# Kernel optimization log

Hardware: AMD Instinct MI355X
Metric: run time of the kernel (lower is better)

The kernel has to match this reference:

```python
import jax, jax.numpy as jnp
import numpy as np

IN_FEATURES = 4096
OUT_FEATURES = 16384

def setup_inputs() -> dict:
    key = jax.random.key(0)
    k1, k2 = jax.random.split(key)
    x = jax.random.normal(k1, (4, 2048, IN_FEATURES), dtype=jnp.float32)
    # init_weights: uniform(-1, 1)
    W = jax.random.uniform(k2, (OUT_FEATURES, IN_FEATURES), dtype=jnp.float32, minval=-1.0, maxval=1.0)
    b = jnp.zeros((OUT_FEATURES,), dtype=jnp.float32)
    return {"x": x, "W": W, "b": b}

def reference(x, W, b):
    # Binarize weights to {-1, 0, +1} via sign, then dense linear: y = x @ sign(W)^T + b
    Wb = jnp.sign(W)
    return jnp.einsum('bsd,od->bso', x, Wb) + b
```

## Files before the change

### kernel.cpp

```cpp
#include <hip/hip_runtime.h>
#include <hip/hip_bf16.h>

#define M_TOT 8192
#define N_TOT 16384
#define K_TOT 4096
#define NT (K_TOT / 64)

typedef int i32x4 __attribute__((ext_vector_type(4)));
typedef int i32x16 __attribute__((ext_vector_type(16)));
typedef __bf16 bf16x8 __attribute__((ext_vector_type(8)));
typedef float f32x4 __attribute__((ext_vector_type(4)));

#define GLOAD_LDS16(g, l)                                                     \
  __builtin_amdgcn_global_load_lds(                                           \
      (__attribute__((address_space(1))) const void*)(g),                     \
      (__attribute__((address_space(3))) void*)(l), 16, 0, 0)

__device__ __forceinline__ ushort f2bf_rne(float f) {
  unsigned u = __float_as_uint(f);
  u += 0x7FFFu + ((u >> 16) & 1u);
  return (ushort)(u >> 16);
}
__device__ __forceinline__ ushort sgn_bf16(float w) {
  return w > 0.f ? (ushort)0x3F80u : (w < 0.f ? (ushort)0xBF80u : (ushort)0u);
}


__global__ void quant_x_kernel(const float* __restrict__ x,
                               char* __restrict__ At, float* __restrict__ s) {
  int row = blockIdx.x;
  int tid = threadIdx.x;
  const float4* xr = (const float4*)(x + (size_t)row * K_TOT + tid * 16);
  float4 v[4];
  float amax = 0.f;
#pragma unroll
  for (int j = 0; j < 4; ++j) {
    v[j] = xr[j];
    amax = fmaxf(amax, fmaxf(fmaxf(fabsf(v[j].x), fabsf(v[j].y)),
                             fmaxf(fabsf(v[j].z), fabsf(v[j].w))));
  }
#pragma unroll
  for (int o = 32; o > 0; o >>= 1) amax = fmaxf(amax, __shfl_xor(amax, o));
  __shared__ float wmax[4];
  if ((tid & 63) == 0) wmax[tid >> 6] = amax;
  __syncthreads();
  amax = fmaxf(fmaxf(wmax[0], wmax[1]), fmaxf(wmax[2], wmax[3]));
  float inv = amax > 0.f ? 127.0f / amax : 0.f;
  if (tid == 0) s[row] = amax * (1.0f / 127.0f);
  int q[16];
#pragma unroll
  for (int j = 0; j < 4; ++j) {
    q[j * 4 + 0] = max(-127, min(127, __float2int_rn(v[j].x * inv)));
    q[j * 4 + 1] = max(-127, min(127, __float2int_rn(v[j].y * inv)));
    q[j * 4 + 2] = max(-127, min(127, __float2int_rn(v[j].z * inv)));
    q[j * 4 + 3] = max(-127, min(127, __float2int_rn(v[j].w * inv)));
  }
  int4 o4;
  int* op = (int*)&o4;
#pragma unroll
  for (int j = 0; j < 4; ++j)
    op[j] = (q[j * 4] & 255) | ((q[j * 4 + 1] & 255) << 8) |
            ((q[j * 4 + 2] & 255) << 16) | ((q[j * 4 + 3] & 255) << 24);
  int r32 = row >> 5, l31 = row & 31;
  int kt = tid >> 2, ks = (tid >> 1) & 1, hi = tid & 1;
  size_t dst = ((size_t)(r32 * 128 + kt * 2 + ks) << 10) + ((hi * 32 + l31) << 4);
  *(int4*)(At + dst) = o4;
}

__global__ void quant_w_kernel(const float* __restrict__ w,
                               char* __restrict__ Bt) {
  int n32 = blockIdx.x;
  int t = threadIdx.x;
#pragma unroll 4
  for (int i = 0; i < 32; ++i) {
    int c = i * 256 + t;
    int kt = c >> 7, ks = (c >> 6) & 1, l = c & 63;
    int n = n32 * 32 + (l & 31);
    int k = kt * 64 + ks * 32 + (l >> 5) * 16;
    const float4* src = (const float4*)(w + (size_t)n * K_TOT + k);
    int4 o4;
    int* op = (int*)&o4;
#pragma unroll
    for (int j = 0; j < 4; ++j) {
      float4 v = src[j];
      int q0 = v.x > 0.f ? 1 : (v.x < 0.f ? -1 : 0);
      int q1 = v.y > 0.f ? 1 : (v.y < 0.f ? -1 : 0);
      int q2 = v.z > 0.f ? 1 : (v.z < 0.f ? -1 : 0);
      int q3 = v.w > 0.f ? 1 : (v.w < 0.f ? -1 : 0);
      op[j] = (q0 & 255) | ((q1 & 255) << 8) | ((q2 & 255) << 16) |
              ((q3 & 255) << 24);
    }
    *(int4*)(Bt + ((size_t)n32 << 17) + ((size_t)c << 4)) = o4;
  }
}

__global__ __launch_bounds__(512, 2) void gemm_i8_big4(
    const char* __restrict__ At, const char* __restrict__ Bt,
    const float* __restrict__ s, const float* __restrict__ bias,
    float* __restrict__ C) {
  __shared__ char lds[4][32768];

  int bid = blockIdx.x;
  int wg = (bid & 7) * 256 + (bid >> 3);
  int bnS = wg >> 8;
  int rem = wg & 255;
  int bm = rem >> 3;
  int bn = bnS * 8 + (rem & 7);
  int rowBase = bm * 256;
  int colBase = bn * 256;

  int t = threadIdx.x;
  int lane = t & 63;
  int wave = t >> 6;
  int wr = wave >> 2;
  int wc = wave & 3;
  int l31 = lane & 31;
  int hi = lane >> 5;

  const char* gAp[2];
  const char* gBp[2];
#pragma unroll
  for (int q = 0; q < 2; ++q) {
    int ss = t + 512 * q;
    int g = ss >> 6;
    int r32l = g >> 1, ks = g & 1;
    int j = ss & 63;
    gAp[q] = At + ((size_t)((bm * 8 + r32l) * 128 + ks) << 10) + (j << 4);
    gBp[q] = Bt + ((size_t)((bn * 8 + r32l) * 128 + ks) << 10) + (j << 4);
  }

  i32x16 acc[4][2] = {};

#define STAGE(kt_, buf_)                                                      \
  {                                                                           \
    size_t _o = (size_t)(kt_) << 11;                                          \
    GLOAD_LDS16(gAp[0] + _o, &lds[buf_][t * 16]);                             \
    GLOAD_LDS16(gAp[1] + _o, &lds[buf_][8192 + t * 16]);                      \
    GLOAD_LDS16(gBp[0] + _o, &lds[buf_][16384 + t * 16]);                     \
    GLOAD_LDS16(gBp[1] + _o, &lds[buf_][24576 + t * 16]);                     \
  }
#define COMPUTE(buf_)                                                         \
  {                                                                           \
    const char* _la = &lds[buf_][0];                                          \
    const char* _lb = _la + 16384;                                            \
    _Pragma("unroll") for (int ks = 0; ks < 2; ++ks) {                        \
      i32x4 bf0 = *(const i32x4*)(_lb + (((wc * 2 + 0) * 2 + ks) << 10) +     \
                                  (lane << 4));                               \
      i32x4 bf1 = *(const i32x4*)(_lb + (((wc * 2 + 1) * 2 + ks) << 10) +     \
                                  (lane << 4));                               \
      _Pragma("unroll") for (int mi = 0; mi < 4; ++mi) {                      \
        i32x4 _af = *(const i32x4*)(_la + (((wr * 4 + mi) * 2 + ks) << 10) +  \
                                    (lane << 4));                             \
        acc[mi][0] = __builtin_amdgcn_mfma_i32_32x32x32_i8(                   \
            _af, bf0, acc[mi][0], 0, 0, 0);                                   \
        acc[mi][1] = __builtin_amdgcn_mfma_i32_32x32x32_i8(                   \
            _af, bf1, acc[mi][1], 0, 0, 0);                                   \
      }                                                                       \
    }                                                                         \
  }

  STAGE(0, 0);
  STAGE(1, 1);
  asm volatile("s_waitcnt vmcnt(4)" ::: "memory");
  __builtin_amdgcn_sched_barrier(0);
  __builtin_amdgcn_s_barrier();
  __builtin_amdgcn_sched_barrier(0);

  for (int tt = 0; tt < NT; ++tt) {
    int buf = tt & 3;
    if (tt + 2 < NT) {
      STAGE(tt + 2, (tt + 2) & 3);
      asm volatile("s_waitcnt vmcnt(4)" ::: "memory");
    } else if (tt + 1 < NT) {
      asm volatile("s_waitcnt vmcnt(0)" ::: "memory");
    }
    COMPUTE(buf);
    __builtin_amdgcn_sched_barrier(0);
    __builtin_amdgcn_s_barrier();
    __builtin_amdgcn_sched_barrier(0);
  }

#undef COMPUTE
#undef STAGE

#pragma unroll
  for (int mi = 0; mi < 4; ++mi) {
#pragma unroll
    for (int ni = 0; ni < 2; ++ni) {
      int gc = colBase + wc * 64 + ni * 32 + l31;
      float bv = bias[gc];
#pragma unroll
      for (int rg = 0; rg < 16; ++rg) {
        int rowIn = (rg & 3) + 8 * (rg >> 2) + 4 * hi;
        int gr = rowBase + wr * 128 + mi * 32 + rowIn;
        C[(size_t)gr * N_TOT + gc] = (float)acc[mi][ni][rg] * s[gr] + bv;
      }
    }
  }
}

__global__ void gemm_fused_kernel(const float* __restrict__ A,
                                  const float* __restrict__ W,
                                  const float* __restrict__ bias,
                                  float* __restrict__ C) {
  __shared__ ushort lsA[128 * 32];
  __shared__ ushort lsB[128 * 32];

  int nwg = gridDim.x;
  int bid = blockIdx.x;
  int wg = (bid & 7) * (nwg >> 3) + (bid >> 3);
  const int NBN = N_TOT / 128;
  int bm = wg / NBN;
  int bn = wg % NBN;
  int rowBase = bm * 128;
  int colBase = bn * 128;

  int t = threadIdx.x;
  int lane = t & 63;
  int wave = t >> 6;
  int wm = (wave >> 1) * 64;
  int wn = (wave & 1) * 64;

  f32x4 acc[4][4] = {};

  int srow = t >> 3;
  int scol = (t & 7) * 4;
  int fr = lane & 15;
  int koff = (lane >> 4) * 8;

  for (int k0 = 0; k0 < K_TOT; k0 += 32) {
    float4 va[4], vb[4];
#pragma unroll
    for (int r = 0; r < 4; ++r) {
      va[r] = *(const float4*)&A[(size_t)(rowBase + r * 32 + srow) * K_TOT + k0 + scol];
      vb[r] = *(const float4*)&W[(size_t)(colBase + r * 32 + srow) * K_TOT + k0 + scol];
    }
    __syncthreads();
#pragma unroll
    for (int r = 0; r < 4; ++r) {
      int e = r * 1024 + t * 4;
      ushort4 oa, ob;
      oa.x = f2bf_rne(va[r].x); oa.y = f2bf_rne(va[r].y);
      oa.z = f2bf_rne(va[r].z); oa.w = f2bf_rne(va[r].w);
      ob.x = sgn_bf16(vb[r].x); ob.y = sgn_bf16(vb[r].y);
      ob.z = sgn_bf16(vb[r].z); ob.w = sgn_bf16(vb[r].w);
      *(ushort4*)&lsA[e] = oa;
      *(ushort4*)&lsB[e] = ob;
    }
    __syncthreads();

    bf16x8 af[4], bfr[4];
#pragma unroll
    for (int i = 0; i < 4; ++i)
      af[i] = *(const bf16x8*)&lsA[(wm + i * 16 + fr) * 32 + koff];
#pragma unroll
    for (int j = 0; j < 4; ++j)
      bfr[j] = *(const bf16x8*)&lsB[(wn + j * 16 + fr) * 32 + koff];

#pragma unroll
    for (int i = 0; i < 4; ++i)
#pragma unroll
      for (int j = 0; j < 4; ++j)
        acc[i][j] = __builtin_amdgcn_mfma_f32_16x16x32_bf16(af[i], bfr[j],
                                                            acc[i][j], 0, 0, 0);
  }

  int orow0 = rowBase + wm + ((lane >> 4) << 2);
  int ocol0 = colBase + wn + (lane & 15);
#pragma unroll
  for (int i = 0; i < 4; ++i) {
#pragma unroll
    for (int j = 0; j < 4; ++j) {
      int col = ocol0 + j * 16;
      float bv = bias[col];
#pragma unroll
      for (int rg = 0; rg < 4; ++rg) {
        int row = orow0 + i * 16 + rg;
        C[(size_t)row * N_TOT + col] = acc[i][j][rg] + bv;
      }
    }
  }
}

extern "C" void kernel_launch(void* const* d_in, const int* in_sizes, int n_in,
                              void* d_out, int out_size, void* d_ws,
                              size_t ws_size, hipStream_t stream) {
  const float* x = (const float*)d_in[0];
  const float* W = (const float*)d_in[1];
  const float* b = (const float*)d_in[2];
  float* out = (float*)d_out;

  const size_t xq_bytes = (size_t)M_TOT * K_TOT;
  const size_t wq_bytes = (size_t)N_TOT * K_TOT;
  const size_t need = xq_bytes + wq_bytes + M_TOT * 4;

  if (ws_size >= need) {
    char* At = (char*)d_ws;
    char* Bt = At + xq_bytes;
    float* s = (float*)(Bt + wq_bytes);
    quant_x_kernel<<<M_TOT, 256, 0, stream>>>(x, At, s);
    quant_w_kernel<<<N_TOT / 32, 256, 0, stream>>>(W, Bt);
    const int nblocks = (M_TOT / 256) * (N_TOT / 256);
    gemm_i8_big4<<<nblocks, 512, 0, stream>>>(At, Bt, s, b, out);
  } else {
    const int nblocks = (M_TOT / 128) * (N_TOT / 128);
    gemm_fused_kernel<<<nblocks, 256, 0, stream>>>(x, W, b, out);
  }
}
```

Baseline: 679.9 us.

## Use 4 fat waves with 128x128 warp tiles in int8 GEMM

```diff
diff --git a/kernel.cpp b/kernel.cpp
--- a/kernel.cpp
+++ b/kernel.cpp
@@ -94,7 +94,7 @@
   }
 }
 
-__global__ __launch_bounds__(512, 2) void gemm_i8_big4(
+__global__ __launch_bounds__(256, 1) void gemm_i8_fat(
     const char* __restrict__ At, const char* __restrict__ Bt,
     const float* __restrict__ s, const float* __restrict__ bias,
     float* __restrict__ C) {
@@ -112,56 +112,60 @@
   int t = threadIdx.x;
   int lane = t & 63;
   int wave = t >> 6;
-  int wr = wave >> 2;
-  int wc = wave & 3;
+  int wr = wave >> 1;
+  int wc = wave & 1;
   int l31 = lane & 31;
   int hi = lane >> 5;
 
-  const char* gAp[2];
-  const char* gBp[2];
-#pragma unroll
-  for (int q = 0; q < 2; ++q) {
-    int ss = t + 512 * q;
-    int g = ss >> 6;
+  const char* gp[8];
+#pragma unroll
+  for (int q = 0; q < 8; ++q) {
+    int ss = t + 256 * q;
+    int g = (ss >> 6) & 15;
     int r32l = g >> 1, ks = g & 1;
     int j = ss & 63;
-    gAp[q] = At + ((size_t)((bm * 8 + r32l) * 128 + ks) << 10) + (j << 4);
-    gBp[q] = Bt + ((size_t)((bn * 8 + r32l) * 128 + ks) << 10) + (j << 4);
-  }
-
-  i32x16 acc[4][2] = {};
+    const char* base =
+        (q < 4) ? At + ((size_t)((bm * 8 + r32l) * 128 + ks) << 10)
+                : Bt + ((size_t)((bn * 8 + r32l) * 128 + ks) << 10);
+    gp[q] = base + (j << 4);
+  }
+
+  i32x16 acc[4][4] = {};
 
 #define STAGE(kt_, buf_)                                                      \
   {                                                                           \
     size_t _o = (size_t)(kt_) << 11;                                          \
-    GLOAD_LDS16(gAp[0] + _o, &lds[buf_][t * 16]);                             \
-    GLOAD_LDS16(gAp[1] + _o, &lds[buf_][8192 + t * 16]);                      \
-    GLOAD_LDS16(gBp[0] + _o, &lds[buf_][16384 + t * 16]);                     \
-    GLOAD_LDS16(gBp[1] + _o, &lds[buf_][24576 + t * 16]);                     \
+    GLOAD_LDS16(gp[0] + _o, &lds[buf_][t * 16]);                              \
+    GLOAD_LDS16(gp[1] + _o, &lds[buf_][4096 + t * 16]);                       \
+    GLOAD_LDS16(gp[2] + _o, &lds[buf_][8192 + t * 16]);                       \
+    GLOAD_LDS16(gp[3] + _o, &lds[buf_][12288 + t * 16]);                      \
+    GLOAD_LDS16(gp[4] + _o, &lds[buf_][16384 + t * 16]);                      \
+    GLOAD_LDS16(gp[5] + _o, &lds[buf_][20480 + t * 16]);                      \
+    GLOAD_LDS16(gp[6] + _o, &lds[buf_][24576 + t * 16]);                      \
+    GLOAD_LDS16(gp[7] + _o, &lds[buf_][28672 + t * 16]);                      \
   }
 #define COMPUTE(buf_)                                                         \
   {                                                                           \
     const char* _la = &lds[buf_][0];                                          \
     const char* _lb = _la + 16384;                                            \
     _Pragma("unroll") for (int ks = 0; ks < 2; ++ks) {                        \
-      i32x4 bf0 = *(const i32x4*)(_lb + (((wc * 2 + 0) * 2 + ks) << 10) +     \
-                                  (lane << 4));                               \
-      i32x4 bf1 = *(const i32x4*)(_lb + (((wc * 2 + 1) * 2 + ks) << 10) +     \
-                                  (lane << 4));                               \
-      _Pragma("unroll") for (int mi = 0; mi < 4; ++mi) {                      \
-        i32x4 _af = *(const i32x4*)(_la + (((wr * 4 + mi) * 2 + ks) << 10) +  \
-                                    (lane << 4));                             \
-        acc[mi][0] = __builtin_amdgcn_mfma_i32_32x32x32_i8(                   \
-            _af, bf0, acc[mi][0], 0, 0, 0);                                   \
-        acc[mi][1] = __builtin_amdgcn_mfma_i32_32x32x32_i8(                   \
-            _af, bf1, acc[mi][1], 0, 0, 0);                                   \
-      }                                                                       \
+      i32x4 af[4], bf[4];                                                     \
+      _Pragma("unroll") for (int mi = 0; mi < 4; ++mi)                        \
+          af[mi] = *(const i32x4*)(_la + (((wr * 4 + mi) * 2 + ks) << 10) +   \
+                                   (lane << 4));                              \
+      _Pragma("unroll") for (int ni = 0; ni < 4; ++ni)                        \
+          bf[ni] = *(const i32x4*)(_lb + (((wc * 4 + ni) * 2 + ks) << 10) +   \
+                                   (lane << 4));                              \
+      _Pragma("unroll") for (int mi = 0; mi < 4; ++mi)                        \
+          _Pragma("unroll") for (int ni = 0; ni < 4; ++ni)                    \
+              acc[mi][ni] = __builtin_amdgcn_mfma_i32_32x32x32_i8(            \
+                  af[mi], bf[ni], acc[mi][ni], 0, 0, 0);                      \
     }                                                                         \
   }
 
   STAGE(0, 0);
   STAGE(1, 1);
-  asm volatile("s_waitcnt vmcnt(4)" ::: "memory");
+  asm volatile("s_waitcnt vmcnt(8)" ::: "memory");
   __builtin_amdgcn_sched_barrier(0);
   __builtin_amdgcn_s_barrier();
   __builtin_amdgcn_sched_barrier(0);
@@ -170,7 +174,7 @@
     int buf = tt & 3;
     if (tt + 2 < NT) {
       STAGE(tt + 2, (tt + 2) & 3);
-      asm volatile("s_waitcnt vmcnt(4)" ::: "memory");
+      asm volatile("s_waitcnt vmcnt(8)" ::: "memory");
     } else if (tt + 1 < NT) {
       asm volatile("s_waitcnt vmcnt(0)" ::: "memory");
     }
@@ -186,8 +190,8 @@
 #pragma unroll
   for (int mi = 0; mi < 4; ++mi) {
 #pragma unroll
-    for (int ni = 0; ni < 2; ++ni) {
-      int gc = colBase + wc * 64 + ni * 32 + l31;
+    for (int ni = 0; ni < 4; ++ni) {
+      int gc = colBase + wc * 128 + ni * 32 + l31;
       float bv = bias[gc];
 #pragma unroll
       for (int rg = 0; rg < 16; ++rg) {
@@ -301,7 +305,7 @@
     quant_x_kernel<<<M_TOT, 256, 0, stream>>>(x, At, s);
     quant_w_kernel<<<N_TOT / 32, 256, 0, stream>>>(W, Bt);
     const int nblocks = (M_TOT / 256) * (N_TOT / 256);
-    gemm_i8_big4<<<nblocks, 512, 0, stream>>>(At, Bt, s, b, out);
+    gemm_i8_fat<<<nblocks, 256, 0, stream>>>(At, Bt, s, b, out);
   } else {
     const int nblocks = (M_TOT / 128) * (N_TOT / 128);
     gemm_fused_kernel<<<nblocks, 256, 0, stream>>>(x, W, b, out);
```

Measured after the change: 690.6 us. Within noise of the previous version (+1.6%).

## Software-pipeline LDS fragment reads with MFMA in int8 GEMM main loop

Applied to the files above, without the earlier changes.

```diff
diff --git a/kernel.cpp b/kernel.cpp
--- a/kernel.cpp
+++ b/kernel.cpp
@@ -94,7 +94,7 @@
   }
 }
 
-__global__ __launch_bounds__(512, 2) void gemm_i8_big4(
+__global__ __launch_bounds__(512, 2) void gemm_i8_pipe(
     const char* __restrict__ At, const char* __restrict__ Bt,
     const float* __restrict__ s, const float* __restrict__ bias,
     float* __restrict__ C) {
@@ -130,6 +130,7 @@
   }
 
   i32x16 acc[4][2] = {};
+  i32x4 Xa[4], Xb[2], Ya[4], Yb[2];
 
 #define STAGE(kt_, buf_)                                                      \
   {                                                                           \
@@ -139,24 +140,27 @@
     GLOAD_LDS16(gBp[0] + _o, &lds[buf_][16384 + t * 16]);                     \
     GLOAD_LDS16(gBp[1] + _o, &lds[buf_][24576 + t * 16]);                     \
   }
-#define COMPUTE(buf_)                                                         \
+#define READF(Adst, Bdst, buf_, ks_)                                          \
   {                                                                           \
     const char* _la = &lds[buf_][0];                                          \
     const char* _lb = _la + 16384;                                            \
-    _Pragma("unroll") for (int ks = 0; ks < 2; ++ks) {                        \
-      i32x4 bf0 = *(const i32x4*)(_lb + (((wc * 2 + 0) * 2 + ks) << 10) +     \
-                                  (lane << 4));                               \
-      i32x4 bf1 = *(const i32x4*)(_lb + (((wc * 2 + 1) * 2 + ks) << 10) +     \
-                                  (lane << 4));                               \
-      _Pragma("unroll") for (int mi = 0; mi < 4; ++mi) {                      \
-        i32x4 _af = *(const i32x4*)(_la + (((wr * 4 + mi) * 2 + ks) << 10) +  \
-                                    (lane << 4));                             \
-        acc[mi][0] = __builtin_amdgcn_mfma_i32_32x32x32_i8(                   \
-            _af, bf0, acc[mi][0], 0, 0, 0);                                   \
-        acc[mi][1] = __builtin_amdgcn_mfma_i32_32x32x32_i8(                   \
-            _af, bf1, acc[mi][1], 0, 0, 0);                                   \
-      }                                                                       \
+    _Pragma("unroll") for (int mi = 0; mi < 4; ++mi)                          \
+        Adst[mi] = *(const i32x4*)(_la + (((wr * 4 + mi) * 2 + (ks_)) << 10) + \
+                                   (lane << 4));                              \
+    _Pragma("unroll") for (int ni = 0; ni < 2; ++ni)                          \
+        Bdst[ni] = *(const i32x4*)(_lb + (((wc * 2 + ni) * 2 + (ks_)) << 10) + \
+                                   (lane << 4));                              \
+  }
+#define MFMACL(Asrc, Bsrc)                                                    \
+  {                                                                           \
+    __builtin_amdgcn_s_setprio(1);                                            \
+    _Pragma("unroll") for (int mi = 0; mi < 4; ++mi) {                        \
+      acc[mi][0] = __builtin_amdgcn_mfma_i32_32x32x32_i8(Asrc[mi], Bsrc[0],   \
+                                                         acc[mi][0], 0, 0, 0); \
+      acc[mi][1] = __builtin_amdgcn_mfma_i32_32x32x32_i8(Asrc[mi], Bsrc[1],   \
+                                                         acc[mi][1], 0, 0, 0); \
     }                                                                         \
+    __builtin_amdgcn_s_setprio(0);                                            \
   }
 
   STAGE(0, 0);
@@ -165,22 +169,27 @@
   __builtin_amdgcn_sched_barrier(0);
   __builtin_amdgcn_s_barrier();
   __builtin_amdgcn_sched_barrier(0);
+  READF(Xa, Xb, 0, 0);
 
   for (int tt = 0; tt < NT; ++tt) {
     int buf = tt & 3;
+    if (tt + 2 < NT) STAGE(tt + 2, (tt + 2) & 3);
+    READF(Ya, Yb, buf, 1);
+    MFMACL(Xa, Xb);
     if (tt + 2 < NT) {
-      STAGE(tt + 2, (tt + 2) & 3);
       asm volatile("s_waitcnt vmcnt(4)" ::: "memory");
     } else if (tt + 1 < NT) {
       asm volatile("s_waitcnt vmcnt(0)" ::: "memory");
     }
-    COMPUTE(buf);
     __builtin_amdgcn_sched_barrier(0);
     __builtin_amdgcn_s_barrier();
     __builtin_amdgcn_sched_barrier(0);
-  }
-
-#undef COMPUTE
+    if (tt + 1 < NT) READF(Xa, Xb, (tt + 1) & 3, 0);
+    MFMACL(Ya, Yb);
+  }
+
+#undef MFMACL
+#undef READF
 #undef STAGE
 
 #pragma unroll
@@ -301,7 +310,7 @@
     quant_x_kernel<<<M_TOT, 256, 0, stream>>>(x, At, s);
     quant_w_kernel<<<N_TOT / 32, 256, 0, stream>>>(W, Bt);
     const int nblocks = (M_TOT / 256) * (N_TOT / 256);
-    gemm_i8_big4<<<nblocks, 512, 0, stream>>>(At, Bt, s, b, out);
+    gemm_i8_pipe<<<nblocks, 512, 0, stream>>>(At, Bt, s, b, out);
   } else {
     const int nblocks = (M_TOT / 128) * (N_TOT / 128);
     gemm_fused_kernel<<<nblocks, 256, 0, stream>>>(x, W, b, out);
```

Result: faster. 664.9 us (-2.2%).
